# Optimization experiments

Hardware: AMD Instinct MI355X
Metric: run time of the kernel (lower is better)

The kernel has to match this reference:

```python
import jax, jax.numpy as jnp
import numpy as np

K = 100000
M = 512

def setup_inputs() -> dict:
    key = jax.random.key(0)
    k1, k2, k3, k4 = jax.random.split(key, 4)
    x = jax.random.normal(k1, (K, M), dtype=jnp.float32)
    # nn.Linear(m, m): weight [m, m], bias [m]
    W = jax.random.normal(k2, (M, M), dtype=jnp.float32) * (1.0 / np.sqrt(M))
    b = jax.random.normal(k3, (M,), dtype=jnp.float32) * 0.01
    # attention vector a: [2m, 1], xavier-normal-like scale
    a = jax.random.normal(k4, (2 * M, 1), dtype=jnp.float32) * np.sqrt(2.0 / (2 * M + 1))
    return {"x": x, "W": W, "b": b, "a": a}

def reference(x, W, b, a):
    # h = Linear(x): [k, m]
    h = x @ W.T + b
    h_mean = jnp.mean(h, axis=0)            # [m]
    a1 = a[:M, 0]                           # [m], applied to h[i]
    a2 = a[M:, 0]                           # [m], applied to h_mean
    # e[i] = a^T cat(h[i], h_mean) -> vectorized as two dot products
    e = h @ a1 + jnp.dot(h_mean, a2)        # [k]
    e = jax.nn.relu(e)
    alpha = jax.nn.softmax(e, axis=0)       # [k]
    # weighted sum of ORIGINAL features (feat = x, pre-linear)
    return jnp.sum(x * alpha[:, None], axis=0)  # [m]
```

## Files before the change

kernel.cpp:

```cpp
#include <hip/hip_runtime.h>
#include <math.h>

#define MM 512
#define KK 100000
#define NB1 1024
#define NW  (NB1 * 4)
#define SSTR 32
#define NOUT 16


__device__ inline float waveSum(float v){
  #pragma unroll
  for(int off = 32; off > 0; off >>= 1) v += __shfl_down(v, off, 64);
  return v;
}
__device__ inline float waveMax(float v){
  #pragma unroll
  for(int off = 32; off > 0; off >>= 1) v = fmaxf(v, __shfl_down(v, off, 64));
  return v;
}
__device__ inline float dot8(float4 x0, float4 x1, float4 v0, float4 v1){
  return x0.x*v0.x + x0.y*v0.y + x0.z*v0.z + x0.w*v0.w
       + x1.x*v1.x + x1.y*v1.y + x1.z*v1.z + x1.w*v1.w;
}
__device__ inline void fma4(float4& acc, float w, float4 x){
  acc.x += w * x.x; acc.y += w * x.y; acc.z += w * x.z; acc.w += w * x.w;
}
__device__ inline void scale4(float4& v, float s){
  v.x *= s; v.y *= s; v.z *= s; v.w *= s;
}

__global__ __launch_bounds__(512) void k_vu(const float* __restrict__ W,
                                            const float* __restrict__ a,
                                            float* __restrict__ v,
                                            float* __restrict__ u){
  int j  = threadIdx.x;
  int k0 = blockIdx.x * 8;
  float pv = 0.f, pu = 0.f;
  #pragma unroll
  for(int kk = 0; kk < 8; kk++){
    float w = W[(size_t)(k0 + kk) * MM + j];
    pv += w * a[k0 + kk];
    pu += w * a[MM + k0 + kk];
  }
  atomicAdd(&v[j], pv);
  atomicAdd(&u[j], pu);
}

__global__ __launch_bounds__(256) void k_pass1o(const float* __restrict__ x,
                                                const float* __restrict__ vv,
                                                const float* __restrict__ uu,
                                                float* __restrict__ s,
                                                float* __restrict__ sumU,
                                                float* __restrict__ pmax,
                                                float* __restrict__ part,
                                                float* __restrict__ zpart){
  __shared__ float lsum[4];
  __shared__ float lmax[4];
  __shared__ float ezs[4];
  __shared__ float lw[2048];
  int tid  = threadIdx.x;
  int lane = tid & 63;
  int wid  = tid >> 6;
  int gw   = blockIdx.x * 4 + wid;

  const float4* v4 = (const float4*)vv;
  const float4* u4 = (const float4*)uu;
  float4 v0 = v4[lane],      v1 = v4[64 + lane];
  float4 u0 = u4[lane],      u1 = u4[64 + lane];
  float accU = 0.f;
  float m_w  = -3.4e38f;
  float Ez   = 0.f;
  float4 E0 = make_float4(0,0,0,0), E1 = make_float4(0,0,0,0);

  int myN = (KK - 1 - gw) / NW + 1;
  int k = 0;
  for(; k + 4 <= myN; k += 4){
    size_t r0 = (size_t)gw + (size_t)(k + 0) * NW;
    size_t r1 = (size_t)gw + (size_t)(k + 1) * NW;
    size_t r2 = (size_t)gw + (size_t)(k + 2) * NW;
    size_t r3 = (size_t)gw + (size_t)(k + 3) * NW;
    const float4* pa = (const float4*)(x + r0 * MM);
    const float4* pb = (const float4*)(x + r1 * MM);
    const float4* pc = (const float4*)(x + r2 * MM);
    const float4* pd = (const float4*)(x + r3 * MM);
    float4 xa0 = pa[lane], xa1 = pa[64 + lane];
    float4 xb0 = pb[lane], xb1 = pb[64 + lane];
    float4 xc0 = pc[lane], xc1 = pc[64 + lane];
    float4 xd0 = pd[lane], xd1 = pd[64 + lane];
    float d0 = dot8(xa0, xa1, v0, v1);  accU += dot8(xa0, xa1, u0, u1);
    float d1 = dot8(xb0, xb1, v0, v1);  accU += dot8(xb0, xb1, u0, u1);
    float d2 = dot8(xc0, xc1, v0, v1);  accU += dot8(xc0, xc1, u0, u1);
    float d3 = dot8(xd0, xd1, v0, v1);  accU += dot8(xd0, xd1, u0, u1);
    #pragma unroll
    for(int off = 1; off < 64; off <<= 1){
      d0 += __shfl_xor(d0, off, 64);
      d1 += __shfl_xor(d1, off, 64);
      d2 += __shfl_xor(d2, off, 64);
      d3 += __shfl_xor(d3, off, 64);
    }
    float g = fmaxf(fmaxf(d0, d1), fmaxf(d2, d3));
    if(g > m_w){
      float sc = __expf(m_w - g);
      scale4(E0, sc); scale4(E1, sc); Ez *= sc;
      m_w = g;
    }
    float w0 = __expf(d0 - m_w);
    float w1 = __expf(d1 - m_w);
    float w2 = __expf(d2 - m_w);
    float w3 = __expf(d3 - m_w);
    Ez += w0 + w1 + w2 + w3;
    fma4(E0, w0, xa0); fma4(E1, w0, xa1);
    fma4(E0, w1, xb0); fma4(E1, w1, xb1);
    fma4(E0, w2, xc0); fma4(E1, w2, xc1);
    fma4(E0, w3, xd0); fma4(E1, w3, xd1);
    float s0 = (lane & 1) ? d1 : d0;
    float s1 = (lane & 1) ? d3 : d2;
    float rr = (lane & 2) ? s1 : s0;
    if(lane < 4) s[gw * SSTR + k + lane] = rr;
  }
  for(; k < myN; k++){
    size_t row = (size_t)gw + (size_t)k * NW;
    const float4* xr = (const float4*)(x + row * MM);
    float4 x0 = xr[lane];
    float4 x1 = xr[64 + lane];
    float d = dot8(x0, x1, v0, v1);
    accU += dot8(x0, x1, u0, u1);
    #pragma unroll
    for(int off = 1; off < 64; off <<= 1) d += __shfl_xor(d, off, 64);
    if(d > m_w){
      float sc = __expf(m_w - d);
      scale4(E0, sc); scale4(E1, sc); Ez *= sc;
      m_w = d;
    }
    float w = __expf(d - m_w);
    Ez += w;
    fma4(E0, w, x0); fma4(E1, w, x1);
    if(lane == 0) s[gw * SSTR + k] = d;
  }

  float us = waveSum(accU);
  if(lane == 0){ lsum[wid] = us; lmax[wid] = m_w; }
  __syncthreads();
  float m_blk = fmaxf(fmaxf(lmax[0], lmax[1]), fmaxf(lmax[2], lmax[3]));
  float sc2 = __expf(m_w - m_blk);
  scale4(E0, sc2); scale4(E1, sc2);
  if(lane == 0) ezs[wid] = Ez * sc2;
  float4* lw4 = (float4*)lw;
  lw4[wid * 128 + lane * 2]     = E0;
  lw4[wid * 128 + lane * 2 + 1] = E1;
  __syncthreads();
  int l = tid >> 2, q = tid & 3;
  float o0 = lw[0*512 + l*8 + q] + lw[1*512 + l*8 + q]
           + lw[2*512 + l*8 + q] + lw[3*512 + l*8 + q];
  float o1 = lw[0*512 + l*8 + 4 + q] + lw[1*512 + l*8 + 4 + q]
           + lw[2*512 + l*8 + 4 + q] + lw[3*512 + l*8 + 4 + q];
  part[(size_t)blockIdx.x * 512 + tid]       = o0;
  part[(size_t)blockIdx.x * 512 + 256 + tid] = o1;
  if(tid == 0){
    atomicAdd(sumU, lsum[0] + lsum[1] + lsum[2] + lsum[3]);
    pmax[blockIdx.x]  = m_blk;
    zpart[blockIdx.x] = ezs[0] + ezs[1] + ezs[2] + ezs[3];
  }
}

__global__ __launch_bounds__(256) void k_corr(const float* __restrict__ x,
                                              const float* __restrict__ s,
                                              const float* __restrict__ b,
                                              const float* __restrict__ a,
                                              const float* __restrict__ sumU,
                                              const float* __restrict__ pmax,
                                              float* __restrict__ part,
                                              const float* __restrict__ zpart,
                                              float* __restrict__ Z){
  __shared__ float red[8];
  __shared__ float czs[4];
  __shared__ float lw[2048];
  int tid  = threadIdx.x;
  int lane = tid & 63;
  int wid  = tid >> 6;
  int gw   = blockIdx.x * 4 + wid;

  float tp = b[tid]       * (a[tid]       + a[MM + tid])
           + b[tid + 256] * (a[tid + 256] + a[MM + tid + 256]);
  float mx = fmaxf(fmaxf(pmax[tid], pmax[tid + 256]),
                   fmaxf(pmax[tid + 512], pmax[tid + 768]));
  float wsum = waveSum(tp);
  mx = waveMax(mx);
  if(lane == 0){ red[wid] = wsum; red[4 + wid] = mx; }
  __syncthreads();
  float c  = sumU[0] * (1.0f / (float)KK) + red[0] + red[1] + red[2] + red[3];
  float mg = fmaxf(fmaxf(red[4], red[5]), fmaxf(red[6], red[7]));
  float M  = fmaxf(0.f, mg + c);
  float eM = __expf(-M);

  float4 C0 = make_float4(0,0,0,0), C1 = make_float4(0,0,0,0);
  float Cz = 0.f;
  int myN = (KK - 1 - gw) / NW + 1;
  const float4* s4 = (const float4*)(s + gw * SSTR);
  #pragma unroll
  for(int g2 = 0; g2 < 7; g2++){
    int kb = g2 * 4;
    if(kb >= myN) break;
    float4 sv = s4[g2];
    {
      int k = kb + 0;
      float t = sv.x + c;
      if(k < myN && t < 0.f){
        float kap = eM - __expf(t - M);
        size_t row = (size_t)gw + (size_t)k * NW;
        const float4* xr = (const float4*)(x + row * MM);
        float4 x0 = xr[lane], x1 = xr[64 + lane];
        fma4(C0, kap, x0); fma4(C1, kap, x1); Cz += kap;
      }
    }
    {
      int k = kb + 1;
      float t = sv.y + c;
      if(k < myN && t < 0.f){
        float kap = eM - __expf(t - M);
        size_t row = (size_t)gw + (size_t)k * NW;
        const float4* xr = (const float4*)(x + row * MM);
        float4 x0 = xr[lane], x1 = xr[64 + lane];
        fma4(C0, kap, x0); fma4(C1, kap, x1); Cz += kap;
      }
    }
    {
      int k = kb + 2;
      float t = sv.z + c;
      if(k < myN && t < 0.f){
        float kap = eM - __expf(t - M);
        size_t row = (size_t)gw + (size_t)k * NW;
        const float4* xr = (const float4*)(x + row * MM);
        float4 x0 = xr[lane], x1 = xr[64 + lane];
        fma4(C0, kap, x0); fma4(C1, kap, x1); Cz += kap;
      }
    }
    {
      int k = kb + 3;
      float t = sv.w + c;
      if(k < myN && t < 0.f){
        float kap = eM - __expf(t - M);
        size_t row = (size_t)gw + (size_t)k * NW;
        const float4* xr = (const float4*)(x + row * MM);
        float4 x0 = xr[lane], x1 = xr[64 + lane];
        fma4(C0, kap, x0); fma4(C1, kap, x1); Cz += kap;
      }
    }
  }

  __syncthreads();
  float4* lw4 = (float4*)lw;
  lw4[wid * 128 + lane * 2]     = C0;
  lw4[wid * 128 + lane * 2 + 1] = C1;
  if(lane == 0) czs[wid] = Cz;
  __syncthreads();
  int l = tid >> 2, q = tid & 3;
  float o0 = lw[0*512 + l*8 + q] + lw[1*512 + l*8 + q]
           + lw[2*512 + l*8 + q] + lw[3*512 + l*8 + q];
  float o1 = lw[0*512 + l*8 + 4 + q] + lw[1*512 + l*8 + 4 + q]
           + lw[2*512 + l*8 + 4 + q] + lw[3*512 + l*8 + 4 + q];
  float scB = __expf(c - M + pmax[blockIdx.x]);
  size_t base = (size_t)blockIdx.x * 512;
  part[base + tid]       = part[base + tid]       * scB + o0;
  part[base + 256 + tid] = part[base + 256 + tid] * scB + o1;
  if(tid == 0)
    atomicAdd(Z, czs[0] + czs[1] + czs[2] + czs[3] + scB * zpart[blockIdx.x]);
}

__global__ __launch_bounds__(256) void k_out(const float* __restrict__ part,
                                             float* __restrict__ acc,
                                             const float* __restrict__ Z,
                                             int* __restrict__ cnt,
                                             float* __restrict__ out){
  __shared__ int lastf;
  int tid = threadIdx.x;
  const float* p = part + (size_t)blockIdx.x * (NB1 / NOUT) * 512;
  float s0 = 0.f, s1 = 0.f;
  #pragma unroll 8
  for(int bb = 0; bb < NB1 / NOUT; bb++){
    s0 += p[bb * 512 + tid];
    s1 += p[bb * 512 + 256 + tid];
  }
  atomicAdd(&acc[tid],       s0);
  atomicAdd(&acc[tid + 256], s1);
  __threadfence();
  if(tid == 0) lastf = (atomicAdd(cnt, 1) == NOUT - 1) ? 1 : 0;
  __syncthreads();
  if(lastf){
    float z = Z[0];
    float v0 = atomicAdd(&acc[tid],       0.0f);
    float v1 = atomicAdd(&acc[tid + 256], 0.0f);
    out[tid]       = v0 / z;
    out[tid + 256] = v1 / z;
  }
}

extern "C" void kernel_launch(void* const* d_in, const int* in_sizes, int n_in,
                              void* d_out, int out_size, void* d_ws, size_t ws_size,
                              hipStream_t stream) {
  const float* x = (const float*)d_in[0];
  const float* W = (const float*)d_in[1];
  const float* b = (const float*)d_in[2];
  const float* a = (const float*)d_in[3];
  float* ws  = (float*)d_ws;
  float* out = (float*)d_out;

  float* v     = ws;
  float* u     = ws + 512;
  float* sumU  = ws + 1024;
  float* Z     = ws + 1025;
  int*   cnt   = (int*)(ws + 1026);
  float* acc   = ws + 1536;
  float* pmax  = ws + 2048;
  float* zpart = ws + 3072;
  float* s     = ws + 4096;
  float* part  = ws + 196608;

  hipMemsetAsync(ws, 0, 2048 * sizeof(float), stream);

  k_vu    <<<64,   512, 0, stream>>>(W, a, v, u);
  k_pass1o<<<NB1,  256, 0, stream>>>(x, v, u, s, sumU, pmax, part, zpart);
  k_corr  <<<NB1,  256, 0, stream>>>(x, s, b, a, sumU, pmax, part, zpart, Z);
  k_out   <<<NOUT, 256, 0, stream>>>(part, acc, Z, cnt, out);
}
```

Baseline: 326.7 us.

## Drop memset and final kernel; fuse output reduction into k_corr via counters

Removes the hipMemsetAsync by having k_vu zero the workspace counters and accumulators, and has k_vu write per-block partials instead of using atomics. Each k_pass1o block sums those partials into shared memory. The separate k_out kernel is folded into k_corr: the last-arriving block of each 64-block group reduces that group's partials, and the last group writes the normalized output. This saves two launches or queue operations at the cost of redundant partial reduction in every pass1 block and a serialized tail reduction.

```diff
diff --git a/kernel.cpp b/kernel.cpp
--- a/kernel.cpp
+++ b/kernel.cpp
@@ -6,7 +6,8 @@
 #define NB1 1024
 #define NW  (NB1 * 4)
 #define SSTR 32
-#define NOUT 16
+#define NVU 16
+#define NCHUNK 16
 
 
 __device__ inline float waveSum(float v){
@@ -32,24 +33,30 @@
 
 __global__ __launch_bounds__(512) void k_vu(const float* __restrict__ W,
                                             const float* __restrict__ a,
-                                            float* __restrict__ v,
-                                            float* __restrict__ u){
+                                            float* __restrict__ vpart,
+                                            float* __restrict__ upart,
+                                            float* __restrict__ ws){
   int j  = threadIdx.x;
-  int k0 = blockIdx.x * 8;
+  int b  = blockIdx.x;
+  int k0 = b * (MM / NVU);
   float pv = 0.f, pu = 0.f;
-  #pragma unroll
-  for(int kk = 0; kk < 8; kk++){
+  #pragma unroll 8
+  for(int kk = 0; kk < MM / NVU; kk++){
     float w = W[(size_t)(k0 + kk) * MM + j];
     pv += w * a[k0 + kk];
     pu += w * a[MM + k0 + kk];
   }
-  atomicAdd(&v[j], pv);
-  atomicAdd(&u[j], pu);
+  vpart[b * MM + j] = pv;
+  upart[b * MM + j] = pu;
+  if(b == 0){
+    if(j < 128) ws[1024 + j] = 0.f;
+    ws[1536 + j] = 0.f;
+  }
 }
 
 __global__ __launch_bounds__(256) void k_pass1o(const float* __restrict__ x,
-                                                const float* __restrict__ vv,
-                                                const float* __restrict__ uu,
+                                                const float* __restrict__ vpart,
+                                                const float* __restrict__ upart,
                                                 float* __restrict__ s,
                                                 float* __restrict__ sumU,
                                                 float* __restrict__ pmax,
@@ -59,13 +66,28 @@
   __shared__ float lmax[4];
   __shared__ float ezs[4];
   __shared__ float lw[2048];
+  __shared__ float vul[1024];
   int tid  = threadIdx.x;
   int lane = tid & 63;
   int wid  = tid >> 6;
   int gw   = blockIdx.x * 4 + wid;
 
-  const float4* v4 = (const float4*)vv;
-  const float4* u4 = (const float4*)uu;
+  #pragma unroll
+  for(int jj = 0; jj < 2; jj++){
+    int j = tid + jj * 256;
+    float sv = 0.f, su = 0.f;
+    #pragma unroll
+    for(int bb = 0; bb < NVU; bb++){
+      sv += vpart[bb * MM + j];
+      su += upart[bb * MM + j];
+    }
+    vul[j]       = sv;
+    vul[512 + j] = su;
+  }
+  __syncthreads();
+
+  const float4* v4 = (const float4*)vul;
+  const float4* u4 = (const float4*)(vul + 512);
   float4 v0 = v4[lane],      v1 = v4[64 + lane];
   float4 u0 = u4[lane],      u1 = u4[64 + lane];
   float accU = 0.f;
@@ -172,10 +194,16 @@
                                               const float* __restrict__ pmax,
                                               float* __restrict__ part,
                                               const float* __restrict__ zpart,
-                                              float* __restrict__ Z){
+                                              float* __restrict__ Z,
+                                              float* __restrict__ acc,
+                                              int* __restrict__ cntc,
+                                              int* __restrict__ cnt2,
+                                              float* __restrict__ out){
   __shared__ float red[8];
   __shared__ float czs[4];
   __shared__ float lw[2048];
+  __shared__ int sArr;
+  __shared__ int sFin;
   int tid  = threadIdx.x;
   int lane = tid & 63;
   int wid  = tid >> 6;
@@ -266,33 +294,35 @@
   part[base + 256 + tid] = part[base + 256 + tid] * scB + o1;
   if(tid == 0)
     atomicAdd(Z, czs[0] + czs[1] + czs[2] + czs[3] + scB * zpart[blockIdx.x]);
-}
-
-__global__ __launch_bounds__(256) void k_out(const float* __restrict__ part,
-                                             float* __restrict__ acc,
-                                             const float* __restrict__ Z,
-                                             int* __restrict__ cnt,
-                                             float* __restrict__ out){
-  __shared__ int lastf;
-  int tid = threadIdx.x;
-  const float* p = part + (size_t)blockIdx.x * (NB1 / NOUT) * 512;
-  float s0 = 0.f, s1 = 0.f;
-  #pragma unroll 8
-  for(int bb = 0; bb < NB1 / NOUT; bb++){
-    s0 += p[bb * 512 + tid];
-    s1 += p[bb * 512 + 256 + tid];
-  }
-  atomicAdd(&acc[tid],       s0);
-  atomicAdd(&acc[tid + 256], s1);
-  __threadfence();
-  if(tid == 0) lastf = (atomicAdd(cnt, 1) == NOUT - 1) ? 1 : 0;
-  __syncthreads();
-  if(lastf){
-    float z = Z[0];
-    float v0 = atomicAdd(&acc[tid],       0.0f);
-    float v1 = atomicAdd(&acc[tid + 256], 0.0f);
-    out[tid]       = v0 / z;
-    out[tid + 256] = v1 / z;
+
+  __syncthreads();
+  if(tid == 0){
+    __threadfence();
+    sArr = atomicAdd(&cntc[blockIdx.x >> 6], 1);
+    if(sArr == 63) __threadfence();
+  }
+  __syncthreads();
+  if(sArr == 63){
+    int g = blockIdx.x >> 6;
+    const float* p = part + (size_t)g * 64 * 512;
+    float r0 = 0.f, r1 = 0.f;
+    #pragma unroll 8
+    for(int bb = 0; bb < 64; bb++){
+      r0 += p[bb * 512 + tid];
+      r1 += p[bb * 512 + 256 + tid];
+    }
+    atomicAdd(&acc[tid],       r0);
+    atomicAdd(&acc[tid + 256], r1);
+    __threadfence();
+    if(tid == 0) sFin = atomicAdd(cnt2, 1);
+    __syncthreads();
+    if(sFin == NCHUNK - 1){
+      float z   = atomicAdd(Z, 0.0f);
+      float v0r = atomicAdd(&acc[tid],       0.0f);
+      float v1r = atomicAdd(&acc[tid + 256], 0.0f);
+      out[tid]       = v0r / z;
+      out[tid + 256] = v1r / z;
+    }
   }
 }
 
@@ -306,21 +336,20 @@
   float* ws  = (float*)d_ws;
   float* out = (float*)d_out;
 
-  float* v     = ws;
-  float* u     = ws + 512;
   float* sumU  = ws + 1024;
   float* Z     = ws + 1025;
-  int*   cnt   = (int*)(ws + 1026);
+  int*   cntc  = (int*)(ws + 1026);
+  int*   cnt2  = (int*)(ws + 1042);
   float* acc   = ws + 1536;
   float* pmax  = ws + 2048;
   float* zpart = ws + 3072;
-  float* s     = ws + 4096;
+  float* vpart = ws + 4096;
+  float* upart = ws + 12288;
+  float* s     = ws + 32768;
   float* part  = ws + 196608;
 
-  hipMemsetAsync(ws, 0, 2048 * sizeof(float), stream);
-
-  k_vu    <<<64,   512, 0, stream>>>(W, a, v, u);
-  k_pass1o<<<NB1,  256, 0, stream>>>(x, v, u, s, sumU, pmax, part, zpart);
-  k_corr  <<<NB1,  256, 0, stream>>>(x, s, b, a, sumU, pmax, part, zpart, Z);
-  k_out   <<<NOUT, 256, 0, stream>>>(part, acc, Z, cnt, out);
-}
+  k_vu    <<<NVU,  512, 0, stream>>>(W, a, vpart, upart, ws);
+  k_pass1o<<<NB1,  256, 0, stream>>>(x, vpart, upart, s, sumU, pmax, part, zpart);
+  k_corr  <<<NB1,  256, 0, stream>>>(x, s, b, a, sumU, pmax, part, zpart, Z,
+                                     acc, cntc, cnt2, out);
+}
```

Result: slower. 344.9 us (+5.6%).

## Predict ReLU-clipped rows in pass one to shrink the correction pass

Applied to the files above, without the earlier changes.

In the first pass, rows whose partial score is below a threshold are guessed to be ReLU-clipped and summed unweighted into a separate accumulator. The correction pass then re-reads x only for rows where the guess disagrees with the true sign of score plus the global offset, rather than for every clipped row. The v/u precompute drops atomics and the memset in favour of per-block partials that pass one reduces itself, with the workspace zeroed inside k_vu. This cuts x traffic in the second pass, at the cost of extra accumulators and LDS reductions in pass one and a dependence on how well the threshold guess matches the data.

```diff
diff --git a/kernel.cpp b/kernel.cpp
--- a/kernel.cpp
+++ b/kernel.cpp
@@ -6,7 +6,9 @@
 #define NB1 1024
 #define NW  (NB1 * 4)
 #define SSTR 32
+#define NVU 16
 #define NOUT 16
+#define THR 0.2f
 
 
 __device__ inline float waveSum(float v){
@@ -26,52 +28,81 @@
 __device__ inline void fma4(float4& acc, float w, float4 x){
   acc.x += w * x.x; acc.y += w * x.y; acc.z += w * x.z; acc.w += w * x.w;
 }
+__device__ inline void add4(float4& acc, float4 x){
+  acc.x += x.x; acc.y += x.y; acc.z += x.z; acc.w += x.w;
+}
 __device__ inline void scale4(float4& v, float s){
   v.x *= s; v.y *= s; v.z *= s; v.w *= s;
 }
 
 __global__ __launch_bounds__(512) void k_vu(const float* __restrict__ W,
                                             const float* __restrict__ a,
-                                            float* __restrict__ v,
-                                            float* __restrict__ u){
+                                            float* __restrict__ vpart,
+                                            float* __restrict__ upart,
+                                            float* __restrict__ ws){
   int j  = threadIdx.x;
-  int k0 = blockIdx.x * 8;
+  int b  = blockIdx.x;
+  int k0 = b * (MM / NVU);
   float pv = 0.f, pu = 0.f;
-  #pragma unroll
-  for(int kk = 0; kk < 8; kk++){
+  #pragma unroll 8
+  for(int kk = 0; kk < MM / NVU; kk++){
     float w = W[(size_t)(k0 + kk) * MM + j];
     pv += w * a[k0 + kk];
     pu += w * a[MM + k0 + kk];
   }
-  atomicAdd(&v[j], pv);
-  atomicAdd(&u[j], pu);
+  vpart[b * MM + j] = pv;
+  upart[b * MM + j] = pu;
+  if(b == 0){
+    if(j < 128) ws[1024 + j] = 0.f;
+    ws[1536 + j] = 0.f;
+  }
 }
 
 __global__ __launch_bounds__(256) void k_pass1o(const float* __restrict__ x,
-                                                const float* __restrict__ vv,
-                                                const float* __restrict__ uu,
+                                                const float* __restrict__ vpart,
+                                                const float* __restrict__ upart,
                                                 float* __restrict__ s,
                                                 float* __restrict__ sumU,
                                                 float* __restrict__ pmax,
-                                                float* __restrict__ part,
-                                                float* __restrict__ zpart){
+                                                float* __restrict__ Epart,
+                                                float* __restrict__ Ppart,
+                                                float* __restrict__ zpart,
+                                                float* __restrict__ nclipa){
   __shared__ float lsum[4];
   __shared__ float lmax[4];
   __shared__ float ezs[4];
+  __shared__ float ncs[4];
   __shared__ float lw[2048];
+  __shared__ float vul[1024];
   int tid  = threadIdx.x;
   int lane = tid & 63;
   int wid  = tid >> 6;
   int gw   = blockIdx.x * 4 + wid;
 
-  const float4* v4 = (const float4*)vv;
-  const float4* u4 = (const float4*)uu;
+  #pragma unroll
+  for(int jj = 0; jj < 2; jj++){
+    int j = tid + jj * 256;
+    float sv = 0.f, su = 0.f;
+    #pragma unroll
+    for(int bb = 0; bb < NVU; bb++){
+      sv += vpart[bb * MM + j];
+      su += upart[bb * MM + j];
+    }
+    vul[j]       = sv;
+    vul[512 + j] = su;
+  }
+  __syncthreads();
+
+  const float4* v4 = (const float4*)vul;
+  const float4* u4 = (const float4*)(vul + 512);
   float4 v0 = v4[lane],      v1 = v4[64 + lane];
   float4 u0 = u4[lane],      u1 = u4[64 + lane];
   float accU = 0.f;
   float m_w  = -3.4e38f;
   float Ez   = 0.f;
+  float ncl  = 0.f;
   float4 E0 = make_float4(0,0,0,0), E1 = make_float4(0,0,0,0);
+  float4 P0 = make_float4(0,0,0,0), P1 = make_float4(0,0,0,0);
 
   int myN = (KK - 1 - gw) / NW + 1;
   int k = 0;
@@ -99,21 +130,25 @@
       d2 += __shfl_xor(d2, off, 64);
       d3 += __shfl_xor(d3, off, 64);
     }
-    float g = fmaxf(fmaxf(d0, d1), fmaxf(d2, d3));
+    bool p0b = d0 < -THR, p1b = d1 < -THR, p2b = d2 < -THR, p3b = d3 < -THR;
+    float e0 = p0b ? -3.4e38f : d0;
+    float e1 = p1b ? -3.4e38f : d1;
+    float e2 = p2b ? -3.4e38f : d2;
+    float e3 = p3b ? -3.4e38f : d3;
+    float g = fmaxf(fmaxf(e0, e1), fmaxf(e2, e3));
     if(g > m_w){
       float sc = __expf(m_w - g);
       scale4(E0, sc); scale4(E1, sc); Ez *= sc;
       m_w = g;
     }
-    float w0 = __expf(d0 - m_w);
-    float w1 = __expf(d1 - m_w);
-    float w2 = __expf(d2 - m_w);
-    float w3 = __expf(d3 - m_w);
-    Ez += w0 + w1 + w2 + w3;
-    fma4(E0, w0, xa0); fma4(E1, w0, xa1);
-    fma4(E0, w1, xb0); fma4(E1, w1, xb1);
-    fma4(E0, w2, xc0); fma4(E1, w2, xc1);
-    fma4(E0, w3, xd0); fma4(E1, w3, xd1);
+    if(p0b){ add4(P0, xa0); add4(P1, xa1); ncl += 1.f; }
+    else   { float w = __expf(d0 - m_w); Ez += w; fma4(E0, w, xa0); fma4(E1, w, xa1); }
+    if(p1b){ add4(P0, xb0); add4(P1, xb1); ncl += 1.f; }
+    else   { float w = __expf(d1 - m_w); Ez += w; fma4(E0, w, xb0); fma4(E1, w, xb1); }
+    if(p2b){ add4(P0, xc0); add4(P1, xc1); ncl += 1.f; }
+    else   { float w = __expf(d2 - m_w); Ez += w; fma4(E0, w, xc0); fma4(E1, w, xc1); }
+    if(p3b){ add4(P0, xd0); add4(P1, xd1); ncl += 1.f; }
+    else   { float w = __expf(d3 - m_w); Ez += w; fma4(E0, w, xd0); fma4(E1, w, xd1); }
     float s0 = (lane & 1) ? d1 : d0;
     float s1 = (lane & 1) ? d3 : d2;
     float rr = (lane & 2) ? s1 : s0;
@@ -128,19 +163,23 @@
     accU += dot8(x0, x1, u0, u1);
     #pragma unroll
     for(int off = 1; off < 64; off <<= 1) d += __shfl_xor(d, off, 64);
-    if(d > m_w){
-      float sc = __expf(m_w - d);
-      scale4(E0, sc); scale4(E1, sc); Ez *= sc;
-      m_w = d;
-    }
-    float w = __expf(d - m_w);
-    Ez += w;
-    fma4(E0, w, x0); fma4(E1, w, x1);
+    if(d < -THR){
+      add4(P0, x0); add4(P1, x1); ncl += 1.f;
+    } else {
+      if(d > m_w){
+        float sc = __expf(m_w - d);
+        scale4(E0, sc); scale4(E1, sc); Ez *= sc;
+        m_w = d;
+      }
+      float w = __expf(d - m_w);
+      Ez += w;
+      fma4(E0, w, x0); fma4(E1, w, x1);
+    }
     if(lane == 0) s[gw * SSTR + k] = d;
   }
 
   float us = waveSum(accU);
-  if(lane == 0){ lsum[wid] = us; lmax[wid] = m_w; }
+  if(lane == 0){ lsum[wid] = us; lmax[wid] = m_w; ncs[wid] = ncl; }
   __syncthreads();
   float m_blk = fmaxf(fmaxf(lmax[0], lmax[1]), fmaxf(lmax[2], lmax[3]));
   float sc2 = __expf(m_w - m_blk);
@@ -155,12 +194,23 @@
            + lw[2*512 + l*8 + q] + lw[3*512 + l*8 + q];
   float o1 = lw[0*512 + l*8 + 4 + q] + lw[1*512 + l*8 + 4 + q]
            + lw[2*512 + l*8 + 4 + q] + lw[3*512 + l*8 + 4 + q];
-  part[(size_t)blockIdx.x * 512 + tid]       = o0;
-  part[(size_t)blockIdx.x * 512 + 256 + tid] = o1;
+  Epart[(size_t)blockIdx.x * 512 + tid]       = o0;
+  Epart[(size_t)blockIdx.x * 512 + 256 + tid] = o1;
+  __syncthreads();
+  lw4[wid * 128 + lane * 2]     = P0;
+  lw4[wid * 128 + lane * 2 + 1] = P1;
+  __syncthreads();
+  float q0 = lw[0*512 + l*8 + q] + lw[1*512 + l*8 + q]
+           + lw[2*512 + l*8 + q] + lw[3*512 + l*8 + q];
+  float q1 = lw[0*512 + l*8 + 4 + q] + lw[1*512 + l*8 + 4 + q]
+           + lw[2*512 + l*8 + 4 + q] + lw[3*512 + l*8 + 4 + q];
+  Ppart[(size_t)blockIdx.x * 512 + tid]       = q0;
+  Ppart[(size_t)blockIdx.x * 512 + 256 + tid] = q1;
   if(tid == 0){
     atomicAdd(sumU, lsum[0] + lsum[1] + lsum[2] + lsum[3]);
-    pmax[blockIdx.x]  = m_blk;
-    zpart[blockIdx.x] = ezs[0] + ezs[1] + ezs[2] + ezs[3];
+    pmax[blockIdx.x]   = m_blk;
+    zpart[blockIdx.x]  = ezs[0] + ezs[1] + ezs[2] + ezs[3];
+    nclipa[blockIdx.x] = ncs[0] + ncs[1] + ncs[2] + ncs[3];
   }
 }
 
@@ -170,8 +220,10 @@
                                               const float* __restrict__ a,
                                               const float* __restrict__ sumU,
                                               const float* __restrict__ pmax,
-                                              float* __restrict__ part,
+                                              float* __restrict__ Epart,
+                                              const float* __restrict__ Ppart,
                                               const float* __restrict__ zpart,
+                                              const float* __restrict__ nclipa,
                                               float* __restrict__ Z){
   __shared__ float red[8];
   __shared__ float czs[4];
@@ -203,44 +255,17 @@
     int kb = g2 * 4;
     if(kb >= myN) break;
     float4 sv = s4[g2];
-    {
-      int k = kb + 0;
-      float t = sv.x + c;
-      if(k < myN && t < 0.f){
-        float kap = eM - __expf(t - M);
-        size_t row = (size_t)gw + (size_t)k * NW;
-        const float4* xr = (const float4*)(x + row * MM);
-        float4 x0 = xr[lane], x1 = xr[64 + lane];
-        fma4(C0, kap, x0); fma4(C1, kap, x1); Cz += kap;
-      }
-    }
-    {
-      int k = kb + 1;
-      float t = sv.y + c;
-      if(k < myN && t < 0.f){
-        float kap = eM - __expf(t - M);
-        size_t row = (size_t)gw + (size_t)k * NW;
-        const float4* xr = (const float4*)(x + row * MM);
-        float4 x0 = xr[lane], x1 = xr[64 + lane];
-        fma4(C0, kap, x0); fma4(C1, kap, x1); Cz += kap;
-      }
-    }
-    {
-      int k = kb + 2;
-      float t = sv.z + c;
-      if(k < myN && t < 0.f){
-        float kap = eM - __expf(t - M);
-        size_t row = (size_t)gw + (size_t)k * NW;
-        const float4* xr = (const float4*)(x + row * MM);
-        float4 x0 = xr[lane], x1 = xr[64 + lane];
-        fma4(C0, kap, x0); fma4(C1, kap, x1); Cz += kap;
-      }
-    }
-    {
-      int k = kb + 3;
-      float t = sv.w + c;
-      if(k < myN && t < 0.f){
-        float kap = eM - __expf(t - M);
+    float svv[4] = {sv.x, sv.y, sv.z, sv.w};
+    #pragma unroll
+    for(int r = 0; r < 4; r++){
+      int k = kb + r;
+      float si = svv[r];
+      float t  = si + c;
+      bool pb  = si < -THR;
+      bool cl  = t  < 0.f;
+      if(k < myN && (pb != cl)){
+        float d  = eM - __expf(t - M);
+        float kap = cl ? d : -d;
         size_t row = (size_t)gw + (size_t)k * NW;
         const float4* xr = (const float4*)(x + row * MM);
         float4 x0 = xr[lane], x1 = xr[64 + lane];
@@ -262,10 +287,13 @@
            + lw[2*512 + l*8 + 4 + q] + lw[3*512 + l*8 + 4 + q];
   float scB = __expf(c - M + pmax[blockIdx.x]);
   size_t base = (size_t)blockIdx.x * 512;
-  part[base + tid]       = part[base + tid]       * scB + o0;
-  part[base + 256 + tid] = part[base + 256 + tid] * scB + o1;
+  Epart[base + tid]       = Epart[base + tid]       * scB
+                          + Ppart[base + tid]       * eM + o0;
+  Epart[base + 256 + tid] = Epart[base + 256 + tid] * scB
+                          + Ppart[base + 256 + tid] * eM + o1;
   if(tid == 0)
-    atomicAdd(Z, czs[0] + czs[1] + czs[2] + czs[3] + scB * zpart[blockIdx.x]);
+    atomicAdd(Z, czs[0] + czs[1] + czs[2] + czs[3]
+                 + scB * zpart[blockIdx.x] + eM * nclipa[blockIdx.x]);
 }
 
 __global__ __launch_bounds__(256) void k_out(const float* __restrict__ part,
@@ -306,21 +334,23 @@
   float* ws  = (float*)d_ws;
   float* out = (float*)d_out;
 
-  float* v     = ws;
-  float* u     = ws + 512;
-  float* sumU  = ws + 1024;
-  float* Z     = ws + 1025;
-  int*   cnt   = (int*)(ws + 1026);
-  float* acc   = ws + 1536;
-  float* pmax  = ws + 2048;
-  float* zpart = ws + 3072;
-  float* s     = ws + 4096;
-  float* part  = ws + 196608;
-
-  hipMemsetAsync(ws, 0, 2048 * sizeof(float), stream);
-
-  k_vu    <<<64,   512, 0, stream>>>(W, a, v, u);
-  k_pass1o<<<NB1,  256, 0, stream>>>(x, v, u, s, sumU, pmax, part, zpart);
-  k_corr  <<<NB1,  256, 0, stream>>>(x, s, b, a, sumU, pmax, part, zpart, Z);
-  k_out   <<<NOUT, 256, 0, stream>>>(part, acc, Z, cnt, out);
-}
+  float* sumU   = ws + 1024;
+  float* Z      = ws + 1025;
+  int*   cnt    = (int*)(ws + 1026);
+  float* acc    = ws + 1536;
+  float* pmax   = ws + 2048;
+  float* zpart  = ws + 3072;
+  float* vpart  = ws + 4096;
+  float* upart  = ws + 12288;
+  float* nclipa = ws + 20480;
+  float* s      = ws + 32768;
+  float* Epart  = ws + 196608;
+  float* Ppart  = ws + 720896;
+
+  k_vu    <<<NVU,  512, 0, stream>>>(W, a, vpart, upart, ws);
+  k_pass1o<<<NB1,  256, 0, stream>>>(x, vpart, upart, s, sumU, pmax,
+                                     Epart, Ppart, zpart, nclipa);
+  k_corr  <<<NB1,  256, 0, stream>>>(x, s, b, a, sumU, pmax,
+                                     Epart, Ppart, zpart, nclipa, Z);
+  k_out   <<<NOUT, 256, 0, stream>>>(Epart, acc, Z, cnt, out);
+}
```

New measurement: 322.5 us. Within noise of the previous version (-1.3%).
